# Kernel tuning notes

Hardware: AMD Instinct MI355X
Metric: run time of the kernel (lower is better)

Reference implementation:

```python
import jax, jax.numpy as jnp
import numpy as np
from jax import lax

CH, GROUP = 32, 8  # channel=32, subchannel=4 -> group=8

def conv2d(x, w, b, pad):
    # x: [B,C,H,W], w: [O,I,kh,kw]
    out = lax.conv_general_dilated(x, w, (1, 1), [(pad, pad), (pad, pad)],
                                   dimension_numbers=("NCHW", "OIHW", "NCHW"))
    return out + b[None, :, None, None]

def pconv(x, w, b):
    # 1x1 conv as einsum; w: [O,I]
    return jnp.einsum("oi,bihw->bohw", w, x) + b[None, :, None, None]

def setup_inputs() -> dict:
    key = jax.random.key(0)
    ks = jax.random.split(key, 32)
    s = 0.05
    d = {
        "x": jax.random.normal(ks[0], (8, CH, 64, 64), jnp.float32),
        "y": jax.random.normal(ks[1], (8, 1, 64, 64), jnp.float32),
        "conv_w": jax.random.normal(ks[2], (CH, CH + GROUP, 3, 3), jnp.float32) * s,
        "conv_b": jax.random.normal(ks[3], (CH,), jnp.float32) * s,
        "score_w": jax.random.normal(ks[4], (1, CH, 3, 3), jnp.float32) * s,
        "score_b": jax.random.normal(ks[5], (1,), jnp.float32) * s,
        "c132_w": jax.random.normal(ks[6], (32, 1, 3, 3), jnp.float32) * s,
        "c132_b": jax.random.normal(ks[7], (32,), jnp.float32) * s,
        "q1_w": jax.random.normal(ks[8], (32, 32), jnp.float32) * s,
        "q1_b": jax.random.normal(ks[9], (32,), jnp.float32) * s,
        "k1_w": jax.random.normal(ks[10], (32, 32), jnp.float32) * s,
        "k1_b": jax.random.normal(ks[11], (32,), jnp.float32) * s,
        "q2_w": jax.random.normal(ks[12], (32, 32), jnp.float32) * s,
        "q2_b": jax.random.normal(ks[13], (32,), jnp.float32) * s,
        "k2_w": jax.random.normal(ks[14], (32, 32), jnp.float32) * s,
        "k2_b": jax.random.normal(ks[15], (32,), jnp.float32) * s,
        "q3_w": jax.random.normal(ks[16], (32, 32), jnp.float32) * s,
        "q3_b": jax.random.normal(ks[17], (32,), jnp.float32) * s,
        "k3_w": jax.random.normal(ks[18], (32, 32), jnp.float32) * s,
        "k3_b": jax.random.normal(ks[19], (32,), jnp.float32) * s,
        "conv6_w": jax.random.normal(ks[20], (32, 64), jnp.float32) * s,
        "conv6_b": jax.random.normal(ks[21], (32,), jnp.float32) * s,
    }
    return d

def reference(x, y, conv_w, conv_b, score_w, score_b, c132_w, c132_b,
              q1_w, q1_b, k1_w, k1_b, q2_w, q2_b, k2_w, k2_b,
              q3_w, q3_b, k3_w, k3_b, conv6_w, conv6_b):
    B, C, H, W = x.shape
    sub = C // GROUP
    # group-wise chunk + interleave y: [x_g0, y, x_g1, y, ...]
    xg = x.reshape(B, GROUP, sub, H, W)
    yb = jnp.broadcast_to(y[:, None], (B, GROUP, 1, H, W))
    x_cat = jnp.concatenate([xg, yb], axis=2).reshape(B, C + GROUP, H, W)
    x1_co = jax.nn.relu(conv2d(x_cat, conv_w, conv_b, 1))        # [B,32,H,W]
    x2_co = conv2d(y, c132_w, c132_b, 1)                          # [B,32,H,W]

    HW = H * W
    x_query1 = pconv(x1_co, q1_w, q1_b).reshape(B, 32, HW)
    x_key1 = pconv(x1_co, k1_w, k1_b).reshape(B, 32, HW)
    x_query2 = pconv(x1_co, q2_w, q2_b).reshape(B, 32, HW)
    x_key2 = pconv(x1_co, k2_w, k2_b).reshape(B, 32, HW)
    y_query = pconv(x2_co, q3_w, q3_b).reshape(B, 32, HW)
    y_key = pconv(x2_co, k3_w, k3_b).reshape(B, 32, HW)

    # spatial attention [B, HW, HW]
    x_hw = jax.nn.softmax(jnp.einsum("bcn,bcm->bnm", x_query1, x_key2), axis=-1)
    # channel attention [B, 32, 32]
    x_c = jax.nn.softmax(jnp.einsum("bcn,bdn->bcd", x_key1, x_query2), axis=-1)

    xy_hw = jnp.einsum("bcn,bnm->bcm", y_query, x_hw).reshape(B, 32, H, W)
    xy_c = jnp.einsum("bcd,bcn->bdn", x_c, y_key).reshape(B, 32, H, W)

    out_final = pconv(jnp.concatenate([xy_hw, xy_c], axis=1), conv6_w, conv6_b)
    x_out = x + out_final
    y_out = y + conv2d(x_out, score_w, score_b, 1)
    return (x_out, y_out)
```

## Files before the change

### kernel.cpp

```cpp
#include <hip/hip_runtime.h>
#include <hip/hip_bf16.h>
#include <math.h>

#define HW 4096

typedef short bf16x8_t __attribute__((ext_vector_type(8)));
typedef float f32x16_t __attribute__((ext_vector_type(16)));
typedef unsigned int u32;
typedef unsigned int u32x4_t __attribute__((ext_vector_type(4)));
typedef int i32x2_t __attribute__((ext_vector_type(2)));

union castu { u32x4_t u; bf16x8_t s; };

static __device__ __forceinline__ unsigned short f2bf(float f){
    union { __bf16 b; unsigned short u; } c; c.b = (__bf16)f; return c.u;
}
static __device__ __forceinline__ u32 pk2(float lo, float hi){
    return ((u32)f2bf(hi) << 16) | (u32)f2bf(lo);
}
static __device__ __forceinline__ bf16x8_t ldb(const unsigned short* p){
    return *reinterpret_cast<const bf16x8_t*>(p);
}
static __device__ __forceinline__ bf16x8_t ld_xs(const unsigned short* p){
    uint2 lo = *(const uint2*)(p);
    uint2 hi = *(const uint2*)(p + 4);
    castu c; c.u = (u32x4_t){lo.x, lo.y, hi.x, hi.y};
    return c.s;
}
static __device__ __forceinline__ f32x16_t mfma32(bf16x8_t a, bf16x8_t b, f32x16_t c){
    return __builtin_amdgcn_mfma_f32_32x32x16_bf16(a, b, c, 0, 0, 0);
}

#define EXP2_MAG  8388608.0f
#define EXP2_BIAS 1064986816.0f

static __device__ __forceinline__ float fexp2(float x){
    return __int_as_float((int)fmaf(x, EXP2_MAG, EXP2_BIAS));
}
static __device__ __forceinline__ u32 pkexp2(float lo, float hi){
    u32 i0 = (u32)(int)fmaf(lo, EXP2_MAG, EXP2_BIAS);
    u32 i1 = (u32)(int)fmaf(hi, EXP2_MAG, EXP2_BIAS);
#if __has_builtin(__builtin_amdgcn_perm)
    return __builtin_amdgcn_perm(i1, i0, 0x07060302u);
#else
    return (i1 & 0xFFFF0000u) | (i0 >> 16);
#endif
}

static __device__ __forceinline__ void cd2bfrag(const u32 P[8], bf16x8_t& b0, bf16x8_t& b1){
    i32x2_t s02 = __builtin_amdgcn_permlane32_swap((int)P[0], (int)P[2], false, false);
    i32x2_t s13 = __builtin_amdgcn_permlane32_swap((int)P[1], (int)P[3], false, false);
    i32x2_t s46 = __builtin_amdgcn_permlane32_swap((int)P[4], (int)P[6], false, false);
    i32x2_t s57 = __builtin_amdgcn_permlane32_swap((int)P[5], (int)P[7], false, false);
    castu c0, c1;
    c0.u = (u32x4_t){ (u32)s02[0], (u32)s13[0], (u32)s02[1], (u32)s13[1] };
    c1.u = (u32x4_t){ (u32)s46[0], (u32)s57[0], (u32)s46[1], (u32)s57[1] };
    b0 = c0.s; b1 = c1.s;
}

#define LOG2E 1.44269504088896340736f


__global__ __launch_bounds__(256, 1) void k_front_mfma(
    const float* __restrict__ x, const float* __restrict__ y,
    const float* __restrict__ conv_w, const float* __restrict__ conv_b,
    const float* __restrict__ c132_w, const float* __restrict__ c132_b,
    const float* __restrict__ q1w, const float* __restrict__ q1b,
    const float* __restrict__ k1w, const float* __restrict__ k1b,
    const float* __restrict__ q2w, const float* __restrict__ q2b,
    const float* __restrict__ k2w, const float* __restrict__ k2b,
    const float* __restrict__ q3w, const float* __restrict__ q3b,
    const float* __restrict__ k3w, const float* __restrict__ k3b,
    float* __restrict__ K1, float* __restrict__ Q2, float* __restrict__ YQ,
    unsigned short* __restrict__ Q1t, unsigned short* __restrict__ K2t,
    unsigned short* __restrict__ YKt)
{
    __shared__ unsigned short xs[4 * 68 * 36];
    __shared__ float ys[4 * 68];
    __shared__ u32 wplane[18 * 4 * 64];
    __shared__ u32 wyplane[4 * 64];
    __shared__ u32 c1plane[4 * 64];

    int tid = threadIdx.x;
    int h0 = blockIdx.x * 2, b = blockIdx.y;

    #pragma unroll
    for (int i = 0; i < 32; ++i){
        int idx = i * 256 + tid;
        int w = idx & 63, ic = (idx >> 6) & 31, dr = idx >> 11;
        int hr = h0 - 1 + dr;
        float v = (hr >= 0 && hr < 64) ? x[((b * 32 + ic) << 12) + (hr << 6) + w] : 0.f;
        xs[(dr * 68 + w + 1) * 36 + ic] = f2bf(v);
    }
    {
        int dr = tid >> 6, ic = tid & 31, side = (tid >> 5) & 1;
        xs[(dr * 68 + (side ? 65 : 0)) * 36 + ic] = 0;
    }
    for (int idx = tid; idx < 272; idx += 256){
        int dr = idx / 68, wp = idx % 68;
        int hr = h0 - 1 + dr, w = wp - 1;
        ys[idx] = (hr >= 0 && hr < 64 && w >= 0 && w < 64) ? y[(b << 12) + (hr << 6) + w] : 0.f;
    }
    for (int e = tid; e < 4608; e += 256){
        int f = e >> 8, wi = (e >> 6) & 3, ln = e & 63;
        int t = f >> 1, j = f & 1, hh = ln >> 5, ll = ln & 31;
        int ic0 = 16 * j + 8 * hh + 2 * wi;
        int co0 = 5 * (ic0 >> 2) + (ic0 & 3);
        int ic1 = ic0 + 1;
        int co1 = 5 * (ic1 >> 2) + (ic1 & 3);
        wplane[e] = pk2(conv_w[ll * 360 + co0 * 9 + t], conv_w[ll * 360 + co1 * 9 + t]);
    }
    {
        int wi = tid >> 6, ln = tid & 63, hh = ln >> 5, ll = ln & 31;
        u32 vy = 0, vc = 0;
        if (hh == 0){
            int t0 = 2 * wi, t1 = 2 * wi + 1;
            float s0 = 0.f, s1 = 0.f;
            #pragma unroll
            for (int g = 0; g < 8; ++g){
                s0 += conv_w[ll * 360 + (5 * g + 4) * 9 + t0];
                s1 += conv_w[ll * 360 + (5 * g + 4) * 9 + t1];
            }
            vy = pk2(s0, s1);
            vc = pk2(c132_w[ll * 9 + t0], c132_w[ll * 9 + t1]);
        } else if (wi == 0){
            float s0 = 0.f;
            #pragma unroll
            for (int g = 0; g < 8; ++g) s0 += conv_w[ll * 360 + (5 * g + 4) * 9 + 8];
            vy = pk2(s0, 0.f);
            vc = pk2(c132_w[ll * 9 + 8], 0.f);
        }
        wyplane[wi * 64 + ln] = vy;
        c1plane[wi * 64 + ln] = vc;
    }
    __syncthreads();

    int lane = tid & 63, wid = tid >> 6;
    int l31 = lane & 31, h = lane >> 5;
    int wr = wid >> 1, toff = (wid & 1) * 32;
    int wpB = toff + l31;

    bf16x8_t wA[18];
    #pragma unroll
    for (int f = 0; f < 18; ++f){
        castu c;
        c.u = (u32x4_t){ wplane[(f * 4 + 0) * 64 + lane], wplane[(f * 4 + 1) * 64 + lane],
                         wplane[(f * 4 + 2) * 64 + lane], wplane[(f * 4 + 3) * 64 + lane] };
        wA[f] = c.s;
    }
    castu wyf, c1f;
    wyf.u = (u32x4_t){ wyplane[lane], wyplane[64 + lane], wyplane[128 + lane], wyplane[192 + lane] };
    c1f.u = (u32x4_t){ c1plane[lane], c1plane[64 + lane], c1plane[128 + lane], c1plane[192 + lane] };

    float yv[8];
    #pragma unroll
    for (int i = 0; i < 8; ++i){
        int tt = 8 * h + i;
        yv[i] = (tt < 9) ? ys[(wr + tt / 3) * 68 + wpB + (tt % 3)] : 0.f;
    }
    castu yf;
    yf.u = (u32x4_t){ pk2(yv[0], yv[1]), pk2(yv[2], yv[3]), pk2(yv[4], yv[5]), pk2(yv[6], yv[7]) };

    f32x16_t accE, accO, accY, acc2;
    #pragma unroll
    for (int r = 0; r < 16; ++r){
        int oc = (r & 3) + 8 * (r >> 2) + 4 * h;
        accE[r] = 0.f; accO[r] = 0.f;
        accY[r] = conv_b[oc]; acc2[r] = c132_b[oc];
    }
    #pragma unroll
    for (int t = 0; t < 9; ++t){
        int base = ((wr + t / 3) * 68 + wpB + (t % 3)) * 36 + 8 * h;
        bf16x8_t b0 = ld_xs(xs + base);
        bf16x8_t b1 = ld_xs(xs + base + 16);
        if (t & 1){
            accO = mfma32(wA[t * 2 + 0], b0, accO);
            accO = mfma32(wA[t * 2 + 1], b1, accO);
        } else {
            accE = mfma32(wA[t * 2 + 0], b0, accE);
            accE = mfma32(wA[t * 2 + 1], b1, accE);
        }
    }
    accY = mfma32(wyf.s, yf.s, accY);
    acc2 = mfma32(c1f.s, yf.s, acc2);

    f32x16_t x1v;
    #pragma unroll
    for (int r = 0; r < 16; ++r){
        float v = accE[r] + accO[r] + accY[r];
        x1v[r] = v > 0.f ? v : 0.f;
    }
    u32 P[8];
    bf16x8_t x1b0, x1b1, x2b0, x2b1;
    #pragma unroll
    for (int t2 = 0; t2 < 8; ++t2) P[t2] = pk2(x1v[2 * t2], x1v[2 * t2 + 1]);
    cd2bfrag(P, x1b0, x1b1);
    #pragma unroll
    for (int t2 = 0; t2 < 8; ++t2) P[t2] = pk2(acc2[2 * t2], acc2[2 * t2 + 1]);
    cd2bfrag(P, x2b0, x2b1);

    int pxg = (h0 + wr) * 64 + toff + l31;
    int tile = ((h0 + wr) << 1) + (wid & 1);
    size_t tb = ((size_t)b * 128 + tile) * 1024;

    {
        f32x16_t a;
        #pragma unroll
        for (int r = 0; r < 16; ++r) a[r] = q1b[(r & 3) + 8 * (r >> 2) + 4 * h];
        const float* p0 = q1w + l31 * 32 + 8 * h;
        castu w0, w1;
        w0.u = (u32x4_t){ pk2(p0[0],p0[1]), pk2(p0[2],p0[3]), pk2(p0[4],p0[5]), pk2(p0[6],p0[7]) };
        w1.u = (u32x4_t){ pk2(p0[16],p0[17]), pk2(p0[18],p0[19]), pk2(p0[20],p0[21]), pk2(p0[22],p0[23]) };
        a = mfma32(w0.s, x1b0, a);
        a = mfma32(w1.s, x1b1, a);
        u32 Q[8];
        #pragma unroll
        for (int t2 = 0; t2 < 8; ++t2) Q[t2] = pk2(a[2 * t2] * LOG2E, a[2 * t2 + 1] * LOG2E);
        bf16x8_t f0, f1; cd2bfrag(Q, f0, f1);
        *(bf16x8_t*)(Q1t + tb + lane * 8)       = f0;
        *(bf16x8_t*)(Q1t + tb + 512 + lane * 8) = f1;
    }
    {
        f32x16_t a;
        #pragma unroll
        for (int r = 0; r < 16; ++r) a[r] = k1b[(r & 3) + 8 * (r >> 2) + 4 * h];
        const float* p0 = k1w + l31 * 32 + 8 * h;
        castu w0, w1;
        w0.u = (u32x4_t){ pk2(p0[0],p0[1]), pk2(p0[2],p0[3]), pk2(p0[4],p0[5]), pk2(p0[6],p0[7]) };
        w1.u = (u32x4_t){ pk2(p0[16],p0[17]), pk2(p0[18],p0[19]), pk2(p0[20],p0[21]), pk2(p0[22],p0[23]) };
        a = mfma32(w0.s, x1b0, a);
        a = mfma32(w1.s, x1b1, a);
        #pragma unroll
        for (int r = 0; r < 16; ++r)
            K1[(b * 32 + (r & 3) + 8 * (r >> 2) + 4 * h) * HW + pxg] = a[r];
    }
    {
        f32x16_t a;
        #pragma unroll
        for (int r = 0; r < 16; ++r) a[r] = q2b[(r & 3) + 8 * (r >> 2) + 4 * h];
        const float* p0 = q2w + l31 * 32 + 8 * h;
        castu w0, w1;
        w0.u = (u32x4_t){ pk2(p0[0],p0[1]), pk2(p0[2],p0[3]), pk2(p0[4],p0[5]), pk2(p0[6],p0[7]) };
        w1.u = (u32x4_t){ pk2(p0[16],p0[17]), pk2(p0[18],p0[19]), pk2(p0[20],p0[21]), pk2(p0[22],p0[23]) };
        a = mfma32(w0.s, x1b0, a);
        a = mfma32(w1.s, x1b1, a);
        #pragma unroll
        for (int r = 0; r < 16; ++r)
            Q2[(b * 32 + (r & 3) + 8 * (r >> 2) + 4 * h) * HW + pxg] = a[r];
    }
    {
        f32x16_t a;
        #pragma unroll
        for (int r = 0; r < 16; ++r) a[r] = k2b[(r & 3) + 8 * (r >> 2) + 4 * h];
        const float* p0 = k2w + l31 * 32 + 8 * h;
        castu w0, w1;
        w0.u = (u32x4_t){ pk2(p0[0],p0[1]), pk2(p0[2],p0[3]), pk2(p0[4],p0[5]), pk2(p0[6],p0[7]) };
        w1.u = (u32x4_t){ pk2(p0[16],p0[17]), pk2(p0[18],p0[19]), pk2(p0[20],p0[21]), pk2(p0[22],p0[23]) };
        a = mfma32(w0.s, x1b0, a);
        a = mfma32(w1.s, x1b1, a);
        u32 Q[8];
        #pragma unroll
        for (int t2 = 0; t2 < 8; ++t2) Q[t2] = pk2(a[2 * t2], a[2 * t2 + 1]);
        bf16x8_t f0, f1; cd2bfrag(Q, f0, f1);
        *(bf16x8_t*)(K2t + tb + lane * 8)       = f0;
        *(bf16x8_t*)(K2t + tb + 512 + lane * 8) = f1;
    }
    {
        f32x16_t a;
        #pragma unroll
        for (int r = 0; r < 16; ++r) a[r] = q3b[(r & 3) + 8 * (r >> 2) + 4 * h];
        const float* p0 = q3w + l31 * 32 + 8 * h;
        castu w0, w1;
        w0.u = (u32x4_t){ pk2(p0[0],p0[1]), pk2(p0[2],p0[3]), pk2(p0[4],p0[5]), pk2(p0[6],p0[7]) };
        w1.u = (u32x4_t){ pk2(p0[16],p0[17]), pk2(p0[18],p0[19]), pk2(p0[20],p0[21]), pk2(p0[22],p0[23]) };
        a = mfma32(w0.s, x2b0, a);
        a = mfma32(w1.s, x2b1, a);
        #pragma unroll
        for (int r = 0; r < 16; ++r)
            YQ[(b * 32 + (r & 3) + 8 * (r >> 2) + 4 * h) * HW + pxg] = a[r];
    }
    {
        f32x16_t a;
        #pragma unroll
        for (int r = 0; r < 16; ++r) a[r] = k3b[(r & 3) + 8 * (r >> 2) + 4 * h];
        const float* p0 = k3w + l31 * 32 + 8 * h;
        castu w0, w1;
        w0.u = (u32x4_t){ pk2(p0[0],p0[1]), pk2(p0[2],p0[3]), pk2(p0[4],p0[5]), pk2(p0[6],p0[7]) };
        w1.u = (u32x4_t){ pk2(p0[16],p0[17]), pk2(p0[18],p0[19]), pk2(p0[20],p0[21]), pk2(p0[22],p0[23]) };
        a = mfma32(w0.s, x2b0, a);
        a = mfma32(w1.s, x2b1, a);
        u32 Q[8];
        #pragma unroll
        for (int t2 = 0; t2 < 8; ++t2) Q[t2] = pk2(a[2 * t2], a[2 * t2 + 1]);
        bf16x8_t f0, f1; cd2bfrag(Q, f0, f1);
        *(bf16x8_t*)(YKt + tb + lane * 8)       = f0;
        *(bf16x8_t*)(YKt + tb + 512 + lane * 8) = f1;
    }
}

__global__ __launch_bounds__(256) void k_chan_part(
    const float* __restrict__ K1, const float* __restrict__ Q2,
    float* __restrict__ Scp)
{
    __shared__ float k1s[128 * 33];
    __shared__ float q2s[128 * 33];
    int b = blockIdx.x & 7;
    int chunk = blockIdx.x >> 3;
    int n0 = chunk * 128;
    int t = threadIdx.x;
    for (int i = 0; i < 16; ++i){
        int idx = i * 256 + t;
        int c = idx >> 7, nl = idx & 127;
        k1s[nl * 33 + c] = K1[(b * 32 + c) * HW + n0 + nl];
        q2s[nl * 33 + c] = Q2[(b * 32 + c) * HW + n0 + nl];
    }
    __syncthreads();
    float acc[4] = {0.f, 0.f, 0.f, 0.f};
    int d = t & 31, c0 = t >> 5;
    for (int nl = 0; nl < 128; ++nl){
        float qv = q2s[nl * 33 + d];
        #pragma unroll
        for (int i = 0; i < 4; ++i)
            acc[i] = fmaf(k1s[nl * 33 + c0 + 8 * i], qv, acc[i]);
    }
    #pragma unroll
    for (int i = 0; i < 4; ++i)
        Scp[(b * 32 + chunk) * 1024 + (c0 + 8 * i) * 32 + d] = acc[i];
}

__global__ __launch_bounds__(1024) void k_chan_fin(
    const float* __restrict__ Scp, const float* __restrict__ c6w,
    float* __restrict__ M2)
{
    __shared__ float pc[32 * 33];
    int b = blockIdx.x;
    int t = threadIdx.x;
    int c = t >> 5, d = t & 31;
    float s = 0.f;
    for (int k = 0; k < 32; ++k) s += Scp[(b * 32 + k) * 1024 + t];
    float mx = s;
    #pragma unroll
    for (int off = 16; off >= 1; off >>= 1) mx = fmaxf(mx, __shfl_xor(mx, off));
    float e = __expf(s - mx);
    float sum = e;
    #pragma unroll
    for (int off = 16; off >= 1; off >>= 1) sum += __shfl_xor(sum, off);
    pc[c * 33 + d] = e / sum;
    __syncthreads();
    int o = t >> 5, cc = t & 31;
    float m2 = 0.f;
    #pragma unroll
    for (int dd = 0; dd < 32; ++dd)
        m2 = fmaf(c6w[o * 64 + 32 + dd], pc[cc * 33 + dd], m2);
    M2[b * 1024 + o * 32 + cc] = m2;
}

__global__ __launch_bounds__(256, 4) void k_stats_mfma(
    const unsigned short* __restrict__ Q1t, const unsigned short* __restrict__ K2t,
    const float* __restrict__ YQ, unsigned short* __restrict__ YQ2)
{
    __shared__ float red[4][16][64];
    __shared__ float ls[32];
    int t = threadIdx.x, wid = t >> 6, lane = t & 63;
    int l31 = lane & 31, h = lane >> 5;
    int b = blockIdx.x & 7, ntile = blockIdx.x >> 3;
    int n0 = ntile * 32;
    size_t qtb = ((size_t)b * 128 + ntile) * 1024;
    bf16x8_t a0 = ldb(Q1t + qtb + lane * 8);
    bf16x8_t a1 = ldb(Q1t + qtb + 512 + lane * 8);
    float accl[16];
    #pragma unroll
    for (int r = 0; r < 16; ++r) accl[r] = 0.f;

    const unsigned short* kp = K2t + ((size_t)b * 128 + (wid << 5)) * 1024 + lane * 8;
    bf16x8_t b0 = ldb(kp), b1 = ldb(kp + 512);
    f32x16_t s_cur;
    #pragma unroll
    for (int r = 0; r < 16; ++r) s_cur[r] = 0.f;
    s_cur = mfma32(a0, b0, s_cur);
    s_cur = mfma32(a1, b1, s_cur);
    kp += 1024;
    bf16x8_t b0n = ldb(kp), b1n = ldb(kp + 512);

    #pragma unroll 4
    for (int i = 0; i < 32; ++i){
        f32x16_t s_nxt;
        #pragma unroll
        for (int r = 0; r < 16; ++r) s_nxt[r] = 0.f;
        __builtin_amdgcn_s_setprio(1);
        s_nxt = mfma32(a0, b0n, s_nxt);
        s_nxt = mfma32(a1, b1n, s_nxt);
        __builtin_amdgcn_s_setprio(0);
        kp += (i < 30) ? 1024 : 0;
        bf16x8_t b0nn = ldb(kp), b1nn = ldb(kp + 512);
        #pragma unroll
        for (int r = 0; r < 16; ++r) accl[r] += fexp2(s_cur[r]);
        s_cur = s_nxt; b0n = b0nn; b1n = b1nn;
    }
    #pragma unroll
    for (int r = 0; r < 16; ++r) red[wid][r][lane] = accl[r];
    __syncthreads();
    if (wid == 0){
        #pragma unroll
        for (int r = 0; r < 16; ++r){
            float v = red[0][r][lane] + red[1][r][lane] + red[2][r][lane] + red[3][r][lane];
            #pragma unroll
            for (int off = 16; off >= 1; off >>= 1) v += __shfl_xor(v, off);
            if (l31 == 0)
                ls[(r & 3) + 8 * (r >> 2) + 4 * h] = 1.0f / v;
        }
    }
    __syncthreads();
    size_t otb = ((size_t)b * 128 + ntile) * 1024;
    #pragma unroll
    for (int p = 0; p < 4; ++p){
        int idx = (p << 8) + t;
        int c = idx >> 5, n = idx & 31;
        size_t g = (size_t)(b * 32 + c) * HW + n0 + n;
        int j = n >> 4, hh = (n >> 3) & 1;
        YQ2[otb + j * 512 + (c + (hh << 5)) * 8 + (n & 7)] = f2bf(YQ[g] * ls[n]);
    }
}

__global__ __launch_bounds__(256, 4) void k_attn_mfma(
    const unsigned short* __restrict__ Q1t, const unsigned short* __restrict__ K2t,
    const unsigned short* __restrict__ YKt, const unsigned short* __restrict__ YQ2,
    const float* __restrict__ M2, const float* __restrict__ c6w, const float* __restrict__ c6b,
    const float* __restrict__ x, float* __restrict__ xout)
{
    __shared__ float red[4][16][64];
    int t = threadIdx.x, wid = t >> 6, lane = t & 63;
    int l31 = lane & 31, h = lane >> 5;
    int b = blockIdx.x & 7, mtile = blockIdx.x >> 3;
    int m0 = mtile * 32;
    size_t ktb = ((size_t)b * 128 + mtile) * 1024;

    bf16x8_t kb0 = ldb(K2t + ktb + lane * 8);
    bf16x8_t kb1 = ldb(K2t + ktb + 512 + lane * 8);

    f32x16_t oacc;
    #pragma unroll
    for (int r = 0; r < 16; ++r) oacc[r] = 0.f;

    const unsigned short* qp = Q1t + ((size_t)b * 128 + (wid << 5)) * 1024 + lane * 8;
    const unsigned short* yp = YQ2 + ((size_t)b * 128 + (wid << 5)) * 1024 + lane * 8;

    bf16x8_t a0 = ldb(qp), a1 = ldb(qp + 512);
    bf16x8_t y0 = ldb(yp), y1 = ldb(yp + 512);
    f32x16_t s_cur;
    #pragma unroll
    for (int r = 0; r < 16; ++r) s_cur[r] = 0.f;
    s_cur = mfma32(a0, kb0, s_cur);
    s_cur = mfma32(a1, kb1, s_cur);
    qp += 1024; yp += 1024;
    bf16x8_t a0n = ldb(qp), a1n = ldb(qp + 512);
    bf16x8_t y0n = ldb(yp), y1n = ldb(yp + 512);

    #pragma unroll 4
    for (int i = 0; i < 32; ++i){
        f32x16_t s_nxt;
        #pragma unroll
        for (int r = 0; r < 16; ++r) s_nxt[r] = 0.f;
        __builtin_amdgcn_s_setprio(1);
        s_nxt = mfma32(a0n, kb0, s_nxt);
        s_nxt = mfma32(a1n, kb1, s_nxt);
        __builtin_amdgcn_s_setprio(0);
        int adv = (i < 30) ? 1024 : 0;
        qp += adv; yp += adv;
        bf16x8_t a0nn = ldb(qp), a1nn = ldb(qp + 512);
        bf16x8_t y0nn = ldb(yp), y1nn = ldb(yp + 512);
        u32 P[8];
        #pragma unroll
        for (int tt = 0; tt < 8; ++tt)
            P[tt] = pkexp2(s_cur[2 * tt], s_cur[2 * tt + 1]);
        bf16x8_t e0, e1;
        cd2bfrag(P, e0, e1);
        __builtin_amdgcn_s_setprio(1);
        oacc = mfma32(y0, e0, oacc);
        oacc = mfma32(y1, e1, oacc);
        __builtin_amdgcn_s_setprio(0);
        s_cur = s_nxt;
        a0n = a0nn; a1n = a1nn;
        y0 = y0n; y1 = y1n; y0n = y0nn; y1n = y1nn;
    }
    #pragma unroll
    for (int r = 0; r < 16; ++r) red[wid][r][lane] = oacc[r];
    __syncthreads();
    if (wid != 0) return;
    #pragma unroll
    for (int r = 0; r < 16; ++r)
        oacc[r] = red[0][r][lane] + red[1][r][lane] + red[2][r][lane] + red[3][r][lane];

    u32 P[8];
    #pragma unroll
    for (int tt = 0; tt < 8; ++tt) P[tt] = pk2(oacc[2 * tt], oacc[2 * tt + 1]);
    bf16x8_t xb0, xb1;
    cd2bfrag(P, xb0, xb1);

    const float* w1p = c6w + l31 * 64;
    const float* m2p = M2 + b * 1024 + l31 * 32;
    int cb0 = 8 * h, cb1 = 16 + 8 * h;
    castu wa0, wa1, ma0, ma1;
    wa0.u = (u32x4_t){ pk2(w1p[cb0], w1p[cb0+1]), pk2(w1p[cb0+2], w1p[cb0+3]),
                       pk2(w1p[cb0+4], w1p[cb0+5]), pk2(w1p[cb0+6], w1p[cb0+7]) };
    wa1.u = (u32x4_t){ pk2(w1p[cb1], w1p[cb1+1]), pk2(w1p[cb1+2], w1p[cb1+3]),
                       pk2(w1p[cb1+4], w1p[cb1+5]), pk2(w1p[cb1+6], w1p[cb1+7]) };
    ma0.u = (u32x4_t){ pk2(m2p[cb0], m2p[cb0+1]), pk2(m2p[cb0+2], m2p[cb0+3]),
                       pk2(m2p[cb0+4], m2p[cb0+5]), pk2(m2p[cb0+6], m2p[cb0+7]) };
    ma1.u = (u32x4_t){ pk2(m2p[cb1], m2p[cb1+1]), pk2(m2p[cb1+2], m2p[cb1+3]),
                       pk2(m2p[cb1+4], m2p[cb1+5]), pk2(m2p[cb1+6], m2p[cb1+7]) };
    bf16x8_t ykb0 = ldb(YKt + ktb + lane * 8);
    bf16x8_t ykb1 = ldb(YKt + ktb + 512 + lane * 8);

    f32x16_t facc;
    #pragma unroll
    for (int r = 0; r < 16; ++r) facc[r] = c6b[(r & 3) + 8 * (r >> 2) + 4 * h];
    facc = mfma32(wa0.s, xb0, facc);
    facc = mfma32(wa1.s, xb1, facc);
    facc = mfma32(ma0.s, ykb0, facc);
    facc = mfma32(ma1.s, ykb1, facc);

    #pragma unroll
    for (int r = 0; r < 16; ++r){
        int o = (r & 3) + 8 * (r >> 2) + 4 * h;
        size_t gi = ((size_t)(b * 32 + o) << 12) + m0 + l31;
        xout[gi] = x[gi] + facc[r];
    }
}

__global__ __launch_bounds__(256) void k_score(
    const float* __restrict__ xout, const float* __restrict__ y,
    const float* __restrict__ sw, const float* __restrict__ sb,
    float* __restrict__ yout)
{
    __shared__ float xs[3][32][66];
    __shared__ float red[4][64];
    int tid = threadIdx.x;
    int b = blockIdx.x & 7, h = blockIdx.x >> 3;
    for (int i = 0; i < 24; ++i){
        int idx = i * 256 + tid;
        int w = idx & 63, ic = (idx >> 6) & 31, dr = idx >> 11;
        int hr = h + dr - 1;
        xs[dr][ic][1 + w] = (hr >= 0 && hr < 64) ? xout[((b * 32 + ic) << 12) + (hr << 6) + w] : 0.f;
    }
    if (tid < 96){ xs[tid >> 5][tid & 31][0] = 0.f; }
    else if (tid < 192){ int u = tid - 96; xs[u >> 5][u & 31][65] = 0.f; }
    __syncthreads();
    int w = tid & 63, icg = tid >> 6;
    float p = 0.f;
    #pragma unroll
    for (int i = 0; i < 8; ++i){
        int ic = icg * 8 + i;
        #pragma unroll
        for (int tap = 0; tap < 9; ++tap)
            p = fmaf(sw[ic * 9 + tap], xs[tap / 3][ic][w + tap % 3], p);
    }
    red[icg][w] = p;
    __syncthreads();
    if (tid < 64){
        int px = (h << 6) + tid;
        yout[b * HW + px] = y[b * HW + px] + sb[0]
                          + red[0][tid] + red[1][tid] + red[2][tid] + red[3][tid];
    }
}

extern "C" void kernel_launch(void* const* d_in, const int* in_sizes, int n_in,
                              void* d_out, int out_size, void* d_ws, size_t ws_size,
                              hipStream_t stream)
{
    (void)in_sizes; (void)n_in; (void)out_size; (void)ws_size;
    const float* x      = (const float*)d_in[0];
    const float* y      = (const float*)d_in[1];
    const float* conv_w = (const float*)d_in[2];
    const float* conv_b = (const float*)d_in[3];
    const float* score_w= (const float*)d_in[4];
    const float* score_b= (const float*)d_in[5];
    const float* c132_w = (const float*)d_in[6];
    const float* c132_b = (const float*)d_in[7];
    const float* q1w = (const float*)d_in[8];  const float* q1b = (const float*)d_in[9];
    const float* k1w = (const float*)d_in[10]; const float* k1b = (const float*)d_in[11];
    const float* q2w = (const float*)d_in[12]; const float* q2b = (const float*)d_in[13];
    const float* k2w = (const float*)d_in[14]; const float* k2b = (const float*)d_in[15];
    const float* q3w = (const float*)d_in[16]; const float* q3b = (const float*)d_in[17];
    const float* k3w = (const float*)d_in[18]; const float* k3b = (const float*)d_in[19];
    const float* c6w = (const float*)d_in[20]; const float* c6b = (const float*)d_in[21];

    float* ws = (float*)d_ws;
    const size_t SZ = 1048576;
    float* Scp = ws;
    float* M2  = ws + 262144;
    float* K1  = ws + 2 * SZ;
    float* Q2  = ws + 3 * SZ;
    float* YQf = ws + 4 * SZ;
    unsigned short* Q1t = (unsigned short*)(ws + 5 * SZ);
    unsigned short* K2t = (unsigned short*)(ws + 5 * SZ + SZ / 2);
    unsigned short* YKt = (unsigned short*)(ws + 6 * SZ);
    unsigned short* YQ2 = (unsigned short*)(ws + 6 * SZ + SZ / 2);

    float* xout = (float*)d_out;
    float* yout = xout + SZ;

    k_front_mfma<<<dim3(32, 8), 256, 0, stream>>>(
        x, y, conv_w, conv_b, c132_w, c132_b,
        q1w, q1b, k1w, k1b, q2w, q2b, k2w, k2b, q3w, q3b, k3w, k3b,
        K1, Q2, YQf, Q1t, K2t, YKt);
    k_chan_part<<<256, 256, 0, stream>>>(K1, Q2, Scp);
    k_chan_fin<<<8, 1024, 0, stream>>>(Scp, c6w, M2);
    k_stats_mfma<<<1024, 256, 0, stream>>>(Q1t, K2t, YQf, YQ2);
    k_attn_mfma<<<1024, 256, 0, stream>>>(Q1t, K2t, YKt, YQ2, M2, c6w, c6b, x, xout);
    k_score<<<512, 256, 0, stream>>>(xout, y, score_w, score_b, yout);
}
```

Measured before the change: 95.29 us.

## Triple-buffer K/Q loads in attention loops and split channel reduction finer

The stats and attention kernels replace a double-buffered software pipeline with a three-deep rotating register buffer, unrolled by three, with the last tile peeled. This gives global loads more lead time before use. Launch bounds drop from 4 to 2 waves per SIMD to leave room for the extra registers, which risks lower occupancy. Separately, the channel-partial kernel uses 64-column chunks over 512 blocks for more parallelism, and the final kernel sums 64 partials.

```diff
diff --git a/kernel.cpp b/kernel.cpp
--- a/kernel.cpp
+++ b/kernel.cpp
@@ -302,22 +302,22 @@
     const float* __restrict__ K1, const float* __restrict__ Q2,
     float* __restrict__ Scp)
 {
-    __shared__ float k1s[128 * 33];
-    __shared__ float q2s[128 * 33];
+    __shared__ float k1s[64 * 33];
+    __shared__ float q2s[64 * 33];
     int b = blockIdx.x & 7;
     int chunk = blockIdx.x >> 3;
-    int n0 = chunk * 128;
+    int n0 = chunk * 64;
     int t = threadIdx.x;
-    for (int i = 0; i < 16; ++i){
+    for (int i = 0; i < 8; ++i){
         int idx = i * 256 + t;
-        int c = idx >> 7, nl = idx & 127;
+        int c = idx >> 6, nl = idx & 63;
         k1s[nl * 33 + c] = K1[(b * 32 + c) * HW + n0 + nl];
         q2s[nl * 33 + c] = Q2[(b * 32 + c) * HW + n0 + nl];
     }
     __syncthreads();
     float acc[4] = {0.f, 0.f, 0.f, 0.f};
     int d = t & 31, c0 = t >> 5;
-    for (int nl = 0; nl < 128; ++nl){
+    for (int nl = 0; nl < 64; ++nl){
         float qv = q2s[nl * 33 + d];
         #pragma unroll
         for (int i = 0; i < 4; ++i)
@@ -325,7 +325,7 @@
     }
     #pragma unroll
     for (int i = 0; i < 4; ++i)
-        Scp[(b * 32 + chunk) * 1024 + (c0 + 8 * i) * 32 + d] = acc[i];
+        Scp[(b * 64 + chunk) * 1024 + (c0 + 8 * i) * 32 + d] = acc[i];
 }
 
 __global__ __launch_bounds__(1024) void k_chan_fin(
@@ -337,7 +337,7 @@
     int t = threadIdx.x;
     int c = t >> 5, d = t & 31;
     float s = 0.f;
-    for (int k = 0; k < 32; ++k) s += Scp[(b * 32 + k) * 1024 + t];
+    for (int k = 0; k < 64; ++k) s += Scp[(b * 64 + k) * 1024 + t];
     float mx = s;
     #pragma unroll
     for (int off = 16; off >= 1; off >>= 1) mx = fmaxf(mx, __shfl_xor(mx, off));
@@ -355,7 +355,7 @@
     M2[b * 1024 + o * 32 + cc] = m2;
 }
 
-__global__ __launch_bounds__(256, 4) void k_stats_mfma(
+__global__ __launch_bounds__(256, 2) void k_stats_mfma(
     const unsigned short* __restrict__ Q1t, const unsigned short* __restrict__ K2t,
     const float* __restrict__ YQ, unsigned short* __restrict__ YQ2)
 {
@@ -372,31 +372,42 @@
     #pragma unroll
     for (int r = 0; r < 16; ++r) accl[r] = 0.f;
 
-    const unsigned short* kp = K2t + ((size_t)b * 128 + (wid << 5)) * 1024 + lane * 8;
-    bf16x8_t b0 = ldb(kp), b1 = ldb(kp + 512);
-    f32x16_t s_cur;
-    #pragma unroll
-    for (int r = 0; r < 16; ++r) s_cur[r] = 0.f;
-    s_cur = mfma32(a0, b0, s_cur);
-    s_cur = mfma32(a1, b1, s_cur);
-    kp += 1024;
-    bf16x8_t b0n = ldb(kp), b1n = ldb(kp + 512);
-
-    #pragma unroll 4
-    for (int i = 0; i < 32; ++i){
-        f32x16_t s_nxt;
-        #pragma unroll
-        for (int r = 0; r < 16; ++r) s_nxt[r] = 0.f;
-        __builtin_amdgcn_s_setprio(1);
-        s_nxt = mfma32(a0, b0n, s_nxt);
-        s_nxt = mfma32(a1, b1n, s_nxt);
-        __builtin_amdgcn_s_setprio(0);
-        kp += (i < 30) ? 1024 : 0;
-        bf16x8_t b0nn = ldb(kp), b1nn = ldb(kp + 512);
+    f32x16_t zz;
+    #pragma unroll
+    for (int r = 0; r < 16; ++r) zz[r] = 0.f;
+
+    const unsigned short* kbase = K2t + ((size_t)b * 128 + (wid << 5)) * 1024 + lane * 8;
+    bf16x8_t b00 = ldb(kbase),        b01 = ldb(kbase + 512);
+    bf16x8_t b10 = ldb(kbase + 1024), b11 = ldb(kbase + 1536);
+    bf16x8_t b20 = ldb(kbase + 2048), b21 = ldb(kbase + 2560);
+    f32x16_t s_cur = mfma32(a0, b00, zz);
+    s_cur = mfma32(a1, b01, s_cur);
+
+    auto body = [&](bf16x8_t& bP0, bf16x8_t& bP1,
+                    bf16x8_t& bN0, bf16x8_t& bN1, int t3){
+        f32x16_t s_nxt = mfma32(a0, bN0, zz);
+        s_nxt = mfma32(a1, bN1, s_nxt);
         #pragma unroll
         for (int r = 0; r < 16; ++r) accl[r] += fexp2(s_cur[r]);
-        s_cur = s_nxt; b0n = b0nn; b1n = b1nn;
-    }
+        const unsigned short* kk = kbase + (size_t)t3 * 1024;
+        bP0 = ldb(kk); bP1 = ldb(kk + 512);
+        s_cur = s_nxt;
+    };
+
+    for (int ii = 0; ii < 30; ii += 3){
+        body(b00, b01, b10, b11, ii + 3);
+        body(b10, b11, b20, b21, ii + 4);
+        body(b20, b21, b00, b01, (ii + 5 > 31) ? 31 : ii + 5);
+    }
+    {
+        f32x16_t s_nxt = mfma32(a0, b10, zz);
+        s_nxt = mfma32(a1, b11, s_nxt);
+        #pragma unroll
+        for (int r = 0; r < 16; ++r) accl[r] += fexp2(s_cur[r]);
+        #pragma unroll
+        for (int r = 0; r < 16; ++r) accl[r] += fexp2(s_nxt[r]);
+    }
+
     #pragma unroll
     for (int r = 0; r < 16; ++r) red[wid][r][lane] = accl[r];
     __syncthreads();
@@ -422,7 +433,7 @@
     }
 }
 
-__global__ __launch_bounds__(256, 4) void k_attn_mfma(
+__global__ __launch_bounds__(256, 2) void k_attn_mfma(
     const unsigned short* __restrict__ Q1t, const unsigned short* __restrict__ K2t,
     const unsigned short* __restrict__ YKt, const unsigned short* __restrict__ YQ2,
     const float* __restrict__ M2, const float* __restrict__ c6w, const float* __restrict__ c6b,
@@ -438,37 +449,27 @@
     bf16x8_t kb0 = ldb(K2t + ktb + lane * 8);
     bf16x8_t kb1 = ldb(K2t + ktb + 512 + lane * 8);
 
-    f32x16_t oacc;
-    #pragma unroll
-    for (int r = 0; r < 16; ++r) oacc[r] = 0.f;
-
-    const unsigned short* qp = Q1t + ((size_t)b * 128 + (wid << 5)) * 1024 + lane * 8;
-    const unsigned short* yp = YQ2 + ((size_t)b * 128 + (wid << 5)) * 1024 + lane * 8;
-
-    bf16x8_t a0 = ldb(qp), a1 = ldb(qp + 512);
-    bf16x8_t y0 = ldb(yp), y1 = ldb(yp + 512);
-    f32x16_t s_cur;
-    #pragma unroll
-    for (int r = 0; r < 16; ++r) s_cur[r] = 0.f;
-    s_cur = mfma32(a0, kb0, s_cur);
-    s_cur = mfma32(a1, kb1, s_cur);
-    qp += 1024; yp += 1024;
-    bf16x8_t a0n = ldb(qp), a1n = ldb(qp + 512);
-    bf16x8_t y0n = ldb(yp), y1n = ldb(yp + 512);
-
-    #pragma unroll 4
-    for (int i = 0; i < 32; ++i){
-        f32x16_t s_nxt;
-        #pragma unroll
-        for (int r = 0; r < 16; ++r) s_nxt[r] = 0.f;
-        __builtin_amdgcn_s_setprio(1);
-        s_nxt = mfma32(a0n, kb0, s_nxt);
-        s_nxt = mfma32(a1n, kb1, s_nxt);
-        __builtin_amdgcn_s_setprio(0);
-        int adv = (i < 30) ? 1024 : 0;
-        qp += adv; yp += adv;
-        bf16x8_t a0nn = ldb(qp), a1nn = ldb(qp + 512);
-        bf16x8_t y0nn = ldb(yp), y1nn = ldb(yp + 512);
+    f32x16_t oacc, zz;
+    #pragma unroll
+    for (int r = 0; r < 16; ++r){ oacc[r] = 0.f; zz[r] = 0.f; }
+
+    const unsigned short* qbase = Q1t + ((size_t)b * 128 + (wid << 5)) * 1024 + lane * 8;
+    const unsigned short* ybase = YQ2 + ((size_t)b * 128 + (wid << 5)) * 1024 + lane * 8;
+
+    bf16x8_t a00 = ldb(qbase),        a01 = ldb(qbase + 512);
+    bf16x8_t a10 = ldb(qbase + 1024), a11 = ldb(qbase + 1536);
+    bf16x8_t a20 = ldb(qbase + 2048), a21 = ldb(qbase + 2560);
+    bf16x8_t y00 = ldb(ybase),        y01 = ldb(ybase + 512);
+    bf16x8_t y10 = ldb(ybase + 1024), y11 = ldb(ybase + 1536);
+    bf16x8_t y20 = ldb(ybase + 2048), y21 = ldb(ybase + 2560);
+
+    f32x16_t s_cur = mfma32(a00, kb0, zz);
+    s_cur = mfma32(a01, kb1, s_cur);
+
+    auto body = [&](bf16x8_t& aP0, bf16x8_t& aP1, bf16x8_t& yP0, bf16x8_t& yP1,
+                    bf16x8_t& aN0, bf16x8_t& aN1, int t3){
+        f32x16_t s_nxt = mfma32(aN0, kb0, zz);
+        s_nxt = mfma32(aN1, kb1, s_nxt);
         u32 P[8];
         #pragma unroll
         for (int tt = 0; tt < 8; ++tt)
@@ -476,13 +477,40 @@
         bf16x8_t e0, e1;
         cd2bfrag(P, e0, e1);
         __builtin_amdgcn_s_setprio(1);
-        oacc = mfma32(y0, e0, oacc);
-        oacc = mfma32(y1, e1, oacc);
+        oacc = mfma32(yP0, e0, oacc);
+        oacc = mfma32(yP1, e1, oacc);
         __builtin_amdgcn_s_setprio(0);
+        const unsigned short* qq = qbase + (size_t)t3 * 1024;
+        const unsigned short* yy = ybase + (size_t)t3 * 1024;
+        aP0 = ldb(qq); aP1 = ldb(qq + 512);
+        yP0 = ldb(yy); yP1 = ldb(yy + 512);
         s_cur = s_nxt;
-        a0n = a0nn; a1n = a1nn;
-        y0 = y0n; y1 = y1n; y0n = y0nn; y1n = y1nn;
-    }
+    };
+
+    for (int ii = 0; ii < 30; ii += 3){
+        body(a00, a01, y00, y01, a10, a11, ii + 3);
+        body(a10, a11, y10, y11, a20, a21, ii + 4);
+        body(a20, a21, y20, y21, a00, a01, (ii + 5 > 31) ? 31 : ii + 5);
+    }
+    {
+        f32x16_t s_nxt = mfma32(a10, kb0, zz);
+        s_nxt = mfma32(a11, kb1, s_nxt);
+        u32 P[8];
+        #pragma unroll
+        for (int tt = 0; tt < 8; ++tt)
+            P[tt] = pkexp2(s_cur[2 * tt], s_cur[2 * tt + 1]);
+        bf16x8_t e0, e1;
+        cd2bfrag(P, e0, e1);
+        oacc = mfma32(y00, e0, oacc);
+        oacc = mfma32(y01, e1, oacc);
+        #pragma unroll
+        for (int tt = 0; tt < 8; ++tt)
+            P[tt] = pkexp2(s_nxt[2 * tt], s_nxt[2 * tt + 1]);
+        cd2bfrag(P, e0, e1);
+        oacc = mfma32(y10, e0, oacc);
+        oacc = mfma32(y11, e1, oacc);
+    }
+
     #pragma unroll
     for (int r = 0; r < 16; ++r) red[wid][r][lane] = oacc[r];
     __syncthreads();
@@ -588,7 +616,7 @@
     float* ws = (float*)d_ws;
     const size_t SZ = 1048576;
     float* Scp = ws;
-    float* M2  = ws + 262144;
+    float* M2  = ws + 524288;
     float* K1  = ws + 2 * SZ;
     float* Q2  = ws + 3 * SZ;
     float* YQf = ws + 4 * SZ;
@@ -604,7 +632,7 @@
         x, y, conv_w, conv_b, c132_w, c132_b,
         q1w, q1b, k1w, k1b, q2w, q2b, k2w, k2b, q3w, q3b, k3w, k3b,
         K1, Q2, YQf, Q1t, K2t, YKt);
-    k_chan_part<<<256, 256, 0, stream>>>(K1, Q2, Scp);
+    k_chan_part<<<512, 256, 0, stream>>>(K1, Q2, Scp);
     k_chan_fin<<<8, 1024, 0, stream>>>(Scp, c6w, M2);
     k_stats_mfma<<<1024, 256, 0, stream>>>(Q1t, K2t, YQf, YQ2);
     k_attn_mfma<<<1024, 256, 0, stream>>>(Q1t, K2t, YKt, YQ2, M2, c6w, c6b, x, xout);
```

Measured after the change: 94.25 us. Within noise of the previous version (-1.1%).
